# Kernel tuning notes

Hardware: AMD Instinct MI355X
Metric: run time of the kernel (lower is better)

The kernel has to match this reference:

```python
import jax, jax.numpy as jnp
import numpy as np

N = 150000
E = 1200000
IN_DIM = 64
HID = 64


def setup_inputs() -> dict:
    key = jax.random.key(0)
    k1, k2, k3, k4 = jax.random.split(key, 4)
    obs = jax.random.normal(k1, (N, IN_DIM), dtype=jnp.float32)
    edge_index = jax.random.randint(k2, (2, E), 0, N, dtype=jnp.int64)
    # GCNConv layer params (Glorot-style scale)
    W1 = jax.random.normal(k3, (IN_DIM, HID), dtype=jnp.float32) / jnp.sqrt(IN_DIM)
    b1 = jnp.zeros((HID,), dtype=jnp.float32)
    W2 = jax.random.normal(k4, (HID, 1), dtype=jnp.float32) / jnp.sqrt(HID)
    b2 = jnp.zeros((1,), dtype=jnp.float32)
    return {"obs": obs, "edge_index": edge_index, "W1": W1, "b1": b1, "W2": W2, "b2": b2}


def gcn_conv(x, W, b, src, dst, n):
    # PyG GCNConv: x' = D^{-1/2} (A + I) D^{-1/2} (x W) + b
    x = x @ W  # [N, F_out]
    # degree with self-loops (edge weight 1)
    deg = jax.ops.segment_sum(jnp.ones((src.shape[0],), x.dtype), dst, num_segments=n) + 1.0
    dinv = jax.lax.rsqrt(deg)  # deg >= 1, safe
    norm = dinv[src] * dinv[dst]  # per-edge norm
    msg = x[src] * norm[:, None]  # gather + scale
    agg = jax.ops.segment_sum(msg, dst, num_segments=n)
    agg = agg + x * (dinv * dinv)[:, None]  # self-loop term
    return agg + b


def reference(obs, edge_index, W1, b1, W2, b2):
    src, dst = edge_index[0], edge_index[1]
    h1 = jax.nn.relu(gcn_conv(obs, W1, b1, src, dst, N))
    h2 = jax.nn.relu(gcn_conv(h1, W2, b2, src, dst, N))
    out = h2.reshape(-1, 15)[:, 3:].reshape(-1)
    return out
```

## Files before the change

### kernel.cpp

```cpp
#include <hip/hip_runtime.h>


#define BK 256
#define NBMAX 640
#define EPB 8192
#define HB 160

typedef unsigned int uint;
typedef unsigned short ushort;
typedef __attribute__((ext_vector_type(8))) short bf16x8_t;
typedef __attribute__((ext_vector_type(4))) float f32x4_t;

static __device__ __forceinline__ ushort f2bf(float x) {
    uint u = __float_as_uint(x);
    u = (u + 0x7FFFu + ((u >> 16) & 1u)) >> 16;
    return (ushort)u;
}

__global__ __launch_bounds__(256) void k_hist(const int* __restrict__ dst, int E, int nb,
                                              int* __restrict__ hist) {
    __shared__ int h[NBMAX];
    const int t = threadIdx.x, b = blockIdx.x;
    for (int j = t; j < nb; j += 256) h[j] = 0;
    __syncthreads();
    const int e0 = b * EPB, e1 = min(e0 + EPB, E);
    for (int e = e0 + t; e < e1; e += 256) atomicAdd(&h[dst[e] >> 8], 1);
    __syncthreads();
    for (int j = t; j < nb; j += 256) hist[j * HB + b] = h[j];
}

__global__ __launch_bounds__(256) void k_cscan1(int* __restrict__ hist, int nblk,
                                                int* __restrict__ colsum) {
    __shared__ int s[256];
    const int j = blockIdx.x, t = threadIdx.x;
    int v = (t < nblk) ? hist[j * HB + t] : 0;
    s[t] = v;
    __syncthreads();
    for (int o = 1; o < 256; o <<= 1) {
        int x = s[t];
        if (t >= o) x += s[t - o];
        __syncthreads();
        s[t] = x;
        __syncthreads();
    }
    if (t < nblk) hist[j * HB + t] = s[t] - v;
    if (t == 255) colsum[j] = s[t];
}

__global__ __launch_bounds__(1024) void k_cscan2(const int* __restrict__ colsum, int nb, int N,
                                                 int* __restrict__ boff, int* __restrict__ rowptr) {
    __shared__ int s[1024];
    const int t = threadIdx.x;
    int v = (t < nb) ? colsum[t] : 0;
    s[t] = v;
    __syncthreads();
    for (int o = 1; o < 1024; o <<= 1) {
        int x = s[t];
        if (t >= o) x += s[t - o];
        __syncthreads();
        s[t] = x;
        __syncthreads();
    }
    if (t < nb) boff[t] = s[t] - v;
    if (t == nb - 1) { boff[nb] = s[t]; rowptr[N] = s[t]; }
}

__global__ __launch_bounds__(256) void k_place(const int* __restrict__ src, const int* __restrict__ dst,
                                               int E, int nb, const int* __restrict__ hist,
                                               const int* __restrict__ boff, uint* __restrict__ ebuf) {
    __shared__ int cur[NBMAX];
    const int t = threadIdx.x, b = blockIdx.x;
    for (int j = t; j < nb; j += 256) cur[j] = boff[j] + hist[j * HB + b];
    __syncthreads();
    const int e0 = b * EPB, e1 = min(e0 + EPB, E);
    for (int e = e0 + t; e < e1; e += 256) {
        int d = dst[e];
        int p = atomicAdd(&cur[d >> 8], 1);
        ebuf[p] = ((uint)(d & 255) << 24) | (uint)src[e];
    }
}

__global__ __launch_bounds__(256) void k_fill3(const uint* __restrict__ ebuf, const int* __restrict__ boff,
                                               int N, int* __restrict__ rowptr, float* __restrict__ dinv,
                                               int* __restrict__ csrc) {
    __shared__ int cnt[BK];
    __shared__ int sc[BK];
    __shared__ int cur[BK];
    const int b = blockIdx.x, v0 = b << 8, t = threadIdx.x;
    const int nv = min(BK, N - v0);
    cnt[t] = 0;
    __syncthreads();
    const int bb = boff[b], be = boff[b + 1];
    for (int j = bb + t; j < be; j += 256) atomicAdd(&cnt[ebuf[j] >> 24], 1);
    __syncthreads();
    const int c = cnt[t];
    if (t < nv) dinv[v0 + t] = rsqrtf((float)c + 1.0f);
    sc[t] = c;
    __syncthreads();
    for (int o = 1; o < 256; o <<= 1) {
        int x = sc[t];
        if (t >= o) x += sc[t - o];
        __syncthreads();
        sc[t] = x;
        __syncthreads();
    }
    const int ex = sc[t] - c + bb;
    if (t < nv) rowptr[v0 + t] = ex;
    cur[t] = ex;
    __syncthreads();
    for (int j = bb + t; j < be; j += 256) {
        uint e = ebuf[j];
        int p = atomicAdd(&cur[e >> 24], 1);
        csrc[p] = (int)(e & 0xFFFFFFu);
    }
}

__global__ __launch_bounds__(256) void k_gemm1(const float* __restrict__ X, const float* __restrict__ W,
                                               const float* __restrict__ dinv, int N,
                                               ushort* __restrict__ Yh) {
    __shared__ __align__(16) ushort Wt[64 * 72];
    const int t = threadIdx.x;

#pragma unroll
    for (int i = 0; i < 4; i++) {
        int idx = t + i * 256;
        int k = idx >> 4;
        int c4 = idx & 15;
        float4 w4 = ((const float4*)W)[idx];
        Wt[(c4 * 4 + 0) * 72 + k] = f2bf(w4.x);
        Wt[(c4 * 4 + 1) * 72 + k] = f2bf(w4.y);
        Wt[(c4 * 4 + 2) * 72 + k] = f2bf(w4.z);
        Wt[(c4 * 4 + 3) * 72 + k] = f2bf(w4.w);
    }
    __syncthreads();

    const int l = t & 63;
    const int lr = l & 15;
    const int g = l >> 4;
    const int rw = blockIdx.x * 64 + (t >> 6) * 16;

    bf16x8_t afr[2];
#pragma unroll
    for (int s = 0; s < 2; s++) {
        const int row = rw + lr;
        float4 xa = make_float4(0.f, 0.f, 0.f, 0.f), xb = xa;
        if (row < N) {
            const float4* xp = (const float4*)(X + (size_t)row * 64 + s * 32 + g * 8);
            xa = xp[0];
            xb = xp[1];
        }
        bf16x8_t af;
        af[0] = (short)f2bf(xa.x); af[1] = (short)f2bf(xa.y);
        af[2] = (short)f2bf(xa.z); af[3] = (short)f2bf(xa.w);
        af[4] = (short)f2bf(xb.x); af[5] = (short)f2bf(xb.y);
        af[6] = (short)f2bf(xb.z); af[7] = (short)f2bf(xb.w);
        afr[s] = af;
    }

    const float4 dv = *(const float4*)(dinv + rw + g * 4);

#pragma unroll
    for (int c = 0; c < 4; c++) {
        f32x4_t acc = {0.f, 0.f, 0.f, 0.f};
#pragma unroll
        for (int s = 0; s < 2; s++) {
            const bf16x8_t bf = *(const bf16x8_t*)&Wt[(c * 16 + lr) * 72 + s * 32 + g * 8];
            acc = __builtin_amdgcn_mfma_f32_16x16x32_bf16(afr[s], bf, acc, 0, 0, 0);
        }
        const int col = c * 16 + lr;
#pragma unroll
        for (int r = 0; r < 4; r++) {
            const int row = rw + g * 4 + r;
            if (row < N) {
                const float sc = (r == 0) ? dv.x : (r == 1) ? dv.y : (r == 2) ? dv.z : dv.w;
                Yh[(size_t)row * 64 + col] = f2bf(acc[r] * sc);
            }
        }
    }
}

__global__ __launch_bounds__(256) void k_agg(const ushort* __restrict__ Yh, const int* __restrict__ rowptr,
                                             const int* __restrict__ csrc, const float* __restrict__ dinv,
                                             const float* __restrict__ b1, const float* __restrict__ W2,
                                             int N, float* __restrict__ zs) {
    int t = blockIdx.x * 256 + threadIdx.x;
    int v = t >> 3;
    if (v >= N) return;
    int li = t & 7;
    const uint4* Y4 = (const uint4*)Yh;
    int start = rowptr[v];
    int cnt = rowptr[v + 1] - start;

    float a[8];
    {
        uint4 m = Y4[(size_t)v * 8 + li];
        a[0] = __uint_as_float(m.x << 16);
        a[1] = __uint_as_float(m.x & 0xFFFF0000u);
        a[2] = __uint_as_float(m.y << 16);
        a[3] = __uint_as_float(m.y & 0xFFFF0000u);
        a[4] = __uint_as_float(m.z << 16);
        a[5] = __uint_as_float(m.z & 0xFFFF0000u);
        a[6] = __uint_as_float(m.w << 16);
        a[7] = __uint_as_float(m.w & 0xFFFF0000u);
    }

    for (int j0 = 0; j0 < cnt; j0 += 8) {
        int rem = cnt - j0;
        int myidx = 0;
        if (li < rem) myidx = csrc[start + j0 + li];
#pragma unroll
        for (int k = 0; k < 8; k++) {
            if (k < rem) {
                int s = __shfl(myidx, k, 8);
                uint4 m = Y4[(size_t)s * 8 + li];
                a[0] += __uint_as_float(m.x << 16);
                a[1] += __uint_as_float(m.x & 0xFFFF0000u);
                a[2] += __uint_as_float(m.y << 16);
                a[3] += __uint_as_float(m.y & 0xFFFF0000u);
                a[4] += __uint_as_float(m.z << 16);
                a[5] += __uint_as_float(m.z & 0xFFFF0000u);
                a[6] += __uint_as_float(m.w << 16);
                a[7] += __uint_as_float(m.w & 0xFFFF0000u);
            }
        }
    }

    float dv = dinv[v];
    float4 ba = ((const float4*)b1)[2 * li], bb = ((const float4*)b1)[2 * li + 1];
    float4 wa = ((const float4*)W2)[2 * li], wb = ((const float4*)W2)[2 * li + 1];
    float p;
    p  = fmaxf(fmaf(dv, a[0], ba.x), 0.f) * wa.x;
    p += fmaxf(fmaf(dv, a[1], ba.y), 0.f) * wa.y;
    p += fmaxf(fmaf(dv, a[2], ba.z), 0.f) * wa.z;
    p += fmaxf(fmaf(dv, a[3], ba.w), 0.f) * wa.w;
    p += fmaxf(fmaf(dv, a[4], bb.x), 0.f) * wb.x;
    p += fmaxf(fmaf(dv, a[5], bb.y), 0.f) * wb.y;
    p += fmaxf(fmaf(dv, a[6], bb.z), 0.f) * wb.z;
    p += fmaxf(fmaf(dv, a[7], bb.w), 0.f) * wb.w;
    p += __shfl_xor(p, 1);
    p += __shfl_xor(p, 2);
    p += __shfl_xor(p, 4);
    if (li == 0) zs[v] = p * dv;
}

__global__ __launch_bounds__(256) void k_out2(const float* __restrict__ zs, const int* __restrict__ rowptr,
                                              const int* __restrict__ csrc, const float* __restrict__ dinv,
                                              const float* __restrict__ b2, int M, float* __restrict__ out) {
    int i = blockIdx.x * 256 + threadIdx.x;
    if (i >= M) return;
    int q = i / 12;
    int c = i - q * 12;
    int v = q * 15 + 3 + c;
    int j = rowptr[v];
    const int end = rowptr[v + 1];
    float s = zs[v];
    for (; j + 4 <= end; j += 4) {
        int i0 = csrc[j], i1 = csrc[j + 1], i2 = csrc[j + 2], i3 = csrc[j + 3];
        s += zs[i0] + zs[i1] + zs[i2] + zs[i3];
    }
    for (; j < end; j++) s += zs[csrc[j]];
    out[i] = fmaxf(fmaf(dinv[v], s, b2[0]), 0.f);
}

extern "C" void kernel_launch(void* const* d_in, const int* in_sizes, int n_in,
                              void* d_out, int out_size, void* d_ws, size_t ws_size,
                              hipStream_t stream) {
    const float* obs = (const float*)d_in[0];
    const int*   ei  = (const int*)d_in[1];
    const float* W1  = (const float*)d_in[2];
    const float* b1  = (const float*)d_in[3];
    const float* W2  = (const float*)d_in[4];
    const float* b2  = (const float*)d_in[5];

    const int N = in_sizes[0] / 64;
    const int E = in_sizes[1] / 2;
    const int M = out_size;
    const int NB = (N + BK - 1) / BK;
    const int NBLK = (E + EPB - 1) / EPB;

    const int* src = ei;
    const int* dst = ei + E;

    ushort* Yh     = (ushort*)d_ws;
    float*  dinv   = (float*)(Yh + (size_t)N * 64);
    float*  zs     = dinv + N;
    int*    rowptr = (int*)(zs + N);
    int*    colsum = rowptr + N + 1;
    int*    boff   = colsum + NBMAX;
    int*    hist   = boff + NBMAX + 1;
    uint*   ebuf   = (uint*)(hist + NBMAX * HB);
    int*    csrc   = (int*)(ebuf + E);

    k_hist  <<<NBLK, 256, 0, stream>>>(dst, E, NB, hist);
    k_cscan1<<<NB, 256, 0, stream>>>(hist, NBLK, colsum);
    k_cscan2<<<1, 1024, 0, stream>>>(colsum, NB, N, boff, rowptr);
    k_place <<<NBLK, 256, 0, stream>>>(src, dst, E, NB, hist, boff, ebuf);
    k_fill3 <<<NB, 256, 0, stream>>>(ebuf, boff, N, rowptr, dinv, csrc);
    k_gemm1 <<<(N + 63) / 64, 256, 0, stream>>>(obs, W1, dinv, N, Yh);
    k_agg   <<<((size_t)N * 8 + 255) / 256, 256, 0, stream>>>(Yh, rowptr, csrc, dinv, b1, W2, N, zs);
    k_out2  <<<(M + 255) / 256, 256, 0, stream>>>(zs, rowptr, csrc, dinv, b2, M, (float*)d_out);
}
```

Baseline: 106.6 us.

## Merge column scans via last-block ticket and stage GEMM output through LDS

The two-kernel scan is folded into one kernel. Each block scans its column, then takes a global atomic ticket, and the last block to finish scans the column sums to produce the bucket offsets. This removes one kernel launch and its dependency gap. Separately, the GEMM epilogue now writes bf16 results into a padded shared tile and stores them as coalesced 16-byte rows instead of scattered 2-byte stores. The cost is extra LDS use, a barrier, and a serial tail for the last scan block.

Result: slower. 140.7 us (+32.0%).

```diff
diff --git a/kernel.cpp b/kernel.cpp
--- a/kernel.cpp
+++ b/kernel.cpp
@@ -18,9 +18,10 @@
 }
 
 __global__ __launch_bounds__(256) void k_hist(const int* __restrict__ dst, int E, int nb,
-                                              int* __restrict__ hist) {
+                                              int* __restrict__ hist, int* __restrict__ ticket) {
     __shared__ int h[NBMAX];
     const int t = threadIdx.x, b = blockIdx.x;
+    if (b == 0 && t == 0) ticket[0] = 0;
     for (int j = t; j < nb; j += 256) h[j] = 0;
     __syncthreads();
     const int e0 = b * EPB, e1 = min(e0 + EPB, E);
@@ -29,9 +30,11 @@
     for (int j = t; j < nb; j += 256) hist[j * HB + b] = h[j];
 }
 
-__global__ __launch_bounds__(256) void k_cscan1(int* __restrict__ hist, int nblk,
-                                                int* __restrict__ colsum) {
+__global__ __launch_bounds__(256) void k_cscan(int* __restrict__ hist, int nblk, int nb, int N,
+                                               int* __restrict__ colsum, int* __restrict__ boff,
+                                               int* __restrict__ rowptr, int* __restrict__ ticket) {
     __shared__ int s[256];
+    __shared__ int lastflag;
     const int j = blockIdx.x, t = threadIdx.x;
     int v = (t < nblk) ? hist[j * HB + t] : 0;
     s[t] = v;
@@ -45,24 +48,29 @@
     }
     if (t < nblk) hist[j * HB + t] = s[t] - v;
     if (t == 255) colsum[j] = s[t];
-}
-
-__global__ __launch_bounds__(1024) void k_cscan2(const int* __restrict__ colsum, int nb, int N,
-                                                 int* __restrict__ boff, int* __restrict__ rowptr) {
-    __shared__ int s[1024];
-    const int t = threadIdx.x;
-    int v = (t < nb) ? colsum[t] : 0;
-    s[t] = v;
-    __syncthreads();
-    for (int o = 1; o < 1024; o <<= 1) {
-        int x = s[t];
-        if (t >= o) x += s[t - o];
-        __syncthreads();
-        s[t] = x;
-        __syncthreads();
-    }
-    if (t < nb) boff[t] = s[t] - v;
-    if (t == nb - 1) { boff[nb] = s[t]; rowptr[N] = s[t]; }
+    __threadfence();
+    if (t == 0) lastflag = (atomicAdd(ticket, 1) == gridDim.x - 1) ? 1 : 0;
+    __syncthreads();
+    if (!lastflag) return;
+
+    int carry = 0;
+    for (int base = 0; base < nb; base += 256) {
+        int idx = base + t;
+        int val = (idx < nb) ? colsum[idx] : 0;
+        __syncthreads();
+        s[t] = val;
+        __syncthreads();
+        for (int o = 1; o < 256; o <<= 1) {
+            int x = s[t];
+            if (t >= o) x += s[t - o];
+            __syncthreads();
+            s[t] = x;
+            __syncthreads();
+        }
+        if (idx < nb) boff[idx] = carry + s[t] - val;
+        carry += s[255];
+    }
+    if (t == 0) { boff[nb] = carry; rowptr[N] = carry; }
 }
 
 __global__ __launch_bounds__(256) void k_place(const int* __restrict__ src, const int* __restrict__ dst,
@@ -119,6 +127,7 @@
                                                const float* __restrict__ dinv, int N,
                                                ushort* __restrict__ Yh) {
     __shared__ __align__(16) ushort Wt[64 * 72];
+    __shared__ __align__(16) ushort Ot[64 * 72];
     const int t = threadIdx.x;
 
 #pragma unroll
@@ -137,7 +146,9 @@
     const int l = t & 63;
     const int lr = l & 15;
     const int g = l >> 4;
-    const int rw = blockIdx.x * 64 + (t >> 6) * 16;
+    const int wv = t >> 6;
+    const int row0 = blockIdx.x * 64;
+    const int rw = row0 + wv * 16;
 
     bf16x8_t afr[2];
 #pragma unroll
@@ -170,12 +181,20 @@
         const int col = c * 16 + lr;
 #pragma unroll
         for (int r = 0; r < 4; r++) {
-            const int row = rw + g * 4 + r;
-            if (row < N) {
-                const float sc = (r == 0) ? dv.x : (r == 1) ? dv.y : (r == 2) ? dv.z : dv.w;
-                Yh[(size_t)row * 64 + col] = f2bf(acc[r] * sc);
-            }
-        }
+            const float sc = (r == 0) ? dv.x : (r == 1) ? dv.y : (r == 2) ? dv.z : dv.w;
+            Ot[(wv * 16 + g * 4 + r) * 72 + col] = f2bf(acc[r] * sc);
+        }
+    }
+    __syncthreads();
+
+#pragma unroll
+    for (int i = 0; i < 2; i++) {
+        int vi = t + i * 256;
+        int row = vi >> 3;
+        int c8 = vi & 7;
+        int grow = row0 + row;
+        if (grow < N)
+            ((uint4*)(Yh + (size_t)grow * 64))[c8] = *(const uint4*)&Ot[row * 72 + c8 * 8];
     }
 }
 
@@ -287,16 +306,16 @@
     int*    rowptr = (int*)(zs + N);
     int*    colsum = rowptr + N + 1;
     int*    boff   = colsum + NBMAX;
-    int*    hist   = boff + NBMAX + 1;
+    int*    ticket = boff + NBMAX + 1;
+    int*    hist   = ticket + 1;
     uint*   ebuf   = (uint*)(hist + NBMAX * HB);
     int*    csrc   = (int*)(ebuf + E);
 
-    k_hist  <<<NBLK, 256, 0, stream>>>(dst, E, NB, hist);
-    k_cscan1<<<NB, 256, 0, stream>>>(hist, NBLK, colsum);
-    k_cscan2<<<1, 1024, 0, stream>>>(colsum, NB, N, boff, rowptr);
-    k_place <<<NBLK, 256, 0, stream>>>(src, dst, E, NB, hist, boff, ebuf);
-    k_fill3 <<<NB, 256, 0, stream>>>(ebuf, boff, N, rowptr, dinv, csrc);
-    k_gemm1 <<<(N + 63) / 64, 256, 0, stream>>>(obs, W1, dinv, N, Yh);
-    k_agg   <<<((size_t)N * 8 + 255) / 256, 256, 0, stream>>>(Yh, rowptr, csrc, dinv, b1, W2, N, zs);
-    k_out2  <<<(M + 255) / 256, 256, 0, stream>>>(zs, rowptr, csrc, dinv, b2, M, (float*)d_out);
-}
+    k_hist <<<NBLK, 256, 0, stream>>>(dst, E, NB, hist, ticket);
+    k_cscan<<<NB, 256, 0, stream>>>(hist, NBLK, NB, N, colsum, boff, rowptr, ticket);
+    k_place<<<NBLK, 256, 0, stream>>>(src, dst, E, NB, hist, boff, ebuf);
+    k_fill3<<<NB, 256, 0, stream>>>(ebuf, boff, N, rowptr, dinv, csrc);
+    k_gemm1<<<(N + 63) / 64, 256, 0, stream>>>(obs, W1, dinv, N, Yh);
+    k_agg  <<<((size_t)N * 8 + 255) / 256, 256, 0, stream>>>(Yh, rowptr, csrc, dinv, b1, W2, N, zs);
+    k_out2 <<<(M + 255) / 256, 256, 0, stream>>>(zs, rowptr, csrc, dinv, b2, M, (float*)d_out);
+}
```
